# Optimization experiments

Measured on AMD Instinct MI355X. Metric: run time of the kernel, lower is better.

## Reference

```python
import jax, jax.numpy as jnp
import numpy as np

N_USERS = 100000
N_ITEMS = 50000
N = N_USERS + N_ITEMS
EMBED = 64
NNZ = 4800000
N_LAYERS = 3


def setup_inputs() -> dict:
    key = jax.random.key(0)
    k1, k2, k3, k4, k5, k6, k7 = jax.random.split(key, 7)
    adj_rows = jax.random.randint(k1, (NNZ,), 0, N, dtype=jnp.int32)
    adj_cols = jax.random.randint(k2, (NNZ,), 0, N, dtype=jnp.int32)
    # symmetric-normalized LightGCN values are small positives
    adj_vals = jax.random.uniform(k3, (NNZ,), dtype=jnp.float32) * (1.0 / 32.0)
    u_emb = jax.random.normal(k4, (N_USERS, EMBED), dtype=jnp.float32) * 0.1
    i_emb = jax.random.normal(k5, (N_ITEMS, EMBED), dtype=jnp.float32) * 0.1
    u_emb_pre = jax.random.normal(k6, (N_USERS, EMBED), dtype=jnp.float32) * 0.1
    i_emb_pre = jax.random.normal(k7, (N_ITEMS, EMBED), dtype=jnp.float32) * 0.1
    return {"adj_rows": adj_rows, "adj_cols": adj_cols, "adj_vals": adj_vals,
            "u_emb": u_emb, "i_emb": i_emb,
            "u_emb_pre": u_emb_pre, "i_emb_pre": i_emb_pre}


def _spmm(rows, cols, vals, x):
    # y = A @ x with A in COO form; gather neighbor rows, scale, scatter-add.
    gathered = x[cols] * vals[:, None]          # [nnz, d]
    return jax.ops.segment_sum(gathered, rows, num_segments=N)


def reference(adj_rows, adj_cols, adj_vals, u_emb, i_emb, u_emb_pre, i_emb_pre):
    ego = jnp.concatenate([u_emb + u_emb_pre, i_emb + i_emb_pre], axis=0)  # [N, d]
    acc = ego  # running sum instead of stacking all layer outputs
    for _ in range(N_LAYERS):
        ego = _spmm(adj_rows, adj_cols, adj_vals, ego)
        acc = acc + ego
    all_emb = acc / (N_LAYERS + 1)  # layer-wise mean
    u_g = all_emb[:N_USERS]
    i_g = all_emb[N_USERS:]
    return (u_g, i_g)
```

## Files before the change

kernel.cpp:

```cpp
#include <hip/hip_runtime.h>

#define N_USERS 100000
#define N_ITEMS 50000
#define N_NODES 150000
#define EMBED 64
#define N_LAYERS 3

#define BSH 8
#define BROWS 256
#define NB ((N_NODES + BROWS - 1) / BROWS)
#define PCHUNK 4096
#define COLMASK 0x3FFFF

__device__ __forceinline__ unsigned short f2bf(float f) {
    unsigned u = __float_as_uint(f);
    return (unsigned short)((u + 0x7FFFu + ((u >> 16) & 1u)) >> 16);
}

__global__ void lgcn_init(const float* __restrict__ u, const float* __restrict__ it,
                          const float* __restrict__ up, const float* __restrict__ ip,
                          unsigned short* __restrict__ egoh, float* __restrict__ acc) {
    int idx = blockIdx.x * blockDim.x + threadIdx.x;
    const int total = N_NODES * EMBED / 4;
    if (idx >= total) return;
    const int uCount = N_USERS * EMBED / 4;
    float4 v;
    if (idx < uCount) {
        float4 a = reinterpret_cast<const float4*>(u)[idx];
        float4 b = reinterpret_cast<const float4*>(up)[idx];
        v = make_float4(a.x + b.x, a.y + b.y, a.z + b.z, a.w + b.w);
    } else {
        int j = idx - uCount;
        float4 a = reinterpret_cast<const float4*>(it)[j];
        float4 b = reinterpret_cast<const float4*>(ip)[j];
        v = make_float4(a.x + b.x, a.y + b.y, a.z + b.z, a.w + b.w);
    }
    reinterpret_cast<float4*>(acc)[idx] = v;
    ushort4 h;
    h.x = f2bf(v.x); h.y = f2bf(v.y); h.z = f2bf(v.z); h.w = f2bf(v.w);
    reinterpret_cast<ushort4*>(egoh)[idx] = h;
}

__global__ void lgcn_cnt(const int* __restrict__ rows, int* __restrict__ Cmat, int nnz) {
    __shared__ int lcnt[NB];
    int wg = blockIdx.x;
    int c0 = wg * PCHUNK;
    int cend = min(c0 + PCHUNK, nnz);
    for (int b = threadIdx.x; b < NB; b += blockDim.x) lcnt[b] = 0;
    __syncthreads();
    for (int e = c0 + threadIdx.x; e < cend; e += blockDim.x)
        atomicAdd(&lcnt[rows[e] >> BSH], 1);
    __syncthreads();
    for (int b = threadIdx.x; b < NB; b += blockDim.x)
        Cmat[(size_t)wg * NB + b] = lcnt[b];
}

__global__ __launch_bounds__(256) void lgcn_colscan(int* __restrict__ Cmat,
                                                    int* __restrict__ colTotal, int nwg) {
    __shared__ int sm[256];
    int b = blockIdx.x;
    int carry = 0;
    for (int c0 = 0; c0 < nwg; c0 += 256) {
        int wg = c0 + threadIdx.x;
        int v = (wg < nwg) ? Cmat[(size_t)wg * NB + b] : 0;
        sm[threadIdx.x] = v;
        __syncthreads();
        for (int off = 1; off < 256; off <<= 1) {
            int t = (threadIdx.x >= (unsigned)off) ? sm[threadIdx.x - off] : 0;
            __syncthreads();
            sm[threadIdx.x] += t;
            __syncthreads();
        }
        if (wg < nwg) Cmat[(size_t)wg * NB + b] = carry + sm[threadIdx.x] - v;
        carry += sm[255];
        __syncthreads();
    }
    if (threadIdx.x == 0) colTotal[b] = carry;
}

__global__ __launch_bounds__(1024) void lgcn_btscan(const int* __restrict__ colTotal,
                                                    int* __restrict__ bucketBase,
                                                    int* __restrict__ rowptr, int nnz) {
    __shared__ int sm[1024];
    int c = (threadIdx.x < NB) ? colTotal[threadIdx.x] : 0;
    sm[threadIdx.x] = c;
    __syncthreads();
    for (int off = 1; off < 1024; off <<= 1) {
        int t = (threadIdx.x >= (unsigned)off) ? sm[threadIdx.x - off] : 0;
        __syncthreads();
        sm[threadIdx.x] += t;
        __syncthreads();
    }
    if (threadIdx.x < NB) bucketBase[threadIdx.x] = sm[threadIdx.x] - c;
    if (threadIdx.x == 0) { bucketBase[NB] = nnz; rowptr[N_NODES] = nnz; }
}

__global__ __launch_bounds__(256) void lgcn_scatter(
        const int* __restrict__ rows, const int* __restrict__ cols,
        const float* __restrict__ vals, const int* __restrict__ Cmat,
        const int* __restrict__ bucketBase, int2* __restrict__ pcvp, int nnz) {
    __shared__ int lcnt[NB];
    __shared__ int gbase[NB];
    __shared__ int sc[256];
    __shared__ int2 ebuf[PCHUNK];
    __shared__ unsigned short bbuf[PCHUNK];
    int wg = blockIdx.x;
    int c0 = wg * PCHUNK;
    int cend = min(c0 + PCHUNK, nnz);
    int n = cend - c0;

    for (int b = threadIdx.x; b < NB; b += 256) lcnt[b] = 0;
    __syncthreads();
    for (int e = c0 + threadIdx.x; e < cend; e += 256)
        atomicAdd(&lcnt[rows[e] >> BSH], 1);
    __syncthreads();

    int carry = 0;
    for (int base = 0; base < NB; base += 256) {
        int b = base + threadIdx.x;
        int v = (b < NB) ? lcnt[b] : 0;
        sc[threadIdx.x] = v;
        __syncthreads();
        for (int off = 1; off < 256; off <<= 1) {
            int t = (threadIdx.x >= (unsigned)off) ? sc[threadIdx.x - off] : 0;
            __syncthreads();
            sc[threadIdx.x] += t;
            __syncthreads();
        }
        if (b < NB) {
            int excl = carry + sc[threadIdx.x] - v;
            gbase[b] = bucketBase[b] + Cmat[(size_t)wg * NB + b] - excl;
            lcnt[b] = excl;
        }
        carry += sc[255];
        __syncthreads();
    }

    for (int e = c0 + threadIdx.x; e < cend; e += 256) {
        int r = rows[e];
        int b = r >> BSH;
        int lpos = atomicAdd(&lcnt[b], 1);
        ebuf[lpos] = make_int2(((r & (BROWS - 1)) << 18) | cols[e], __float_as_int(vals[e]));
        bbuf[lpos] = (unsigned short)b;
    }
    __syncthreads();

    for (int t = threadIdx.x; t < n; t += 256) {
        int b = bbuf[t];
        pcvp[gbase[b] + t] = ebuf[t];
    }
}

__global__ __launch_bounds__(BROWS) void lgcn_bsort(const int2* __restrict__ pcvp,
                                                    const int* __restrict__ bucketBase,
                                                    int* __restrict__ rowptr,
                                                    int2* __restrict__ cv) {
    __shared__ int sm[BROWS];
    __shared__ int cur[BROWS];
    int b = blockIdx.x;
    int beg = bucketBase[b];
    int end = bucketBase[b + 1];
    sm[threadIdx.x] = 0;
    __syncthreads();
    for (int i = beg + threadIdx.x; i < end; i += BROWS)
        atomicAdd(&sm[((unsigned)pcvp[i].x) >> 18], 1);
    __syncthreads();
    int c = sm[threadIdx.x];
    for (int off = 1; off < BROWS; off <<= 1) {
        int t = (threadIdx.x >= (unsigned)off) ? sm[threadIdx.x - off] : 0;
        __syncthreads();
        sm[threadIdx.x] += t;
        __syncthreads();
    }
    int excl = sm[threadIdx.x] - c;
    cur[threadIdx.x] = beg + excl;
    int node = b * BROWS + (int)threadIdx.x;
    if (node < N_NODES) rowptr[node] = beg + excl;
    __syncthreads();
    for (int i = beg + threadIdx.x; i < end; i += BROWS) {
        int2 p = pcvp[i];
        int rl = ((unsigned)p.x) >> 18;
        int pos = atomicAdd(&cur[rl], 1);
        cv[pos] = make_int2(p.x & COLMASK, p.y);
    }
}

template <bool WRITE_EGO>
__global__ __launch_bounds__(256) void lgcn_spmm_quad(
        const int* __restrict__ rowptr, const int2* __restrict__ cv,
        const unsigned short* __restrict__ x, unsigned short* __restrict__ ego_out,
        float* __restrict__ acc, float scale) {
    int row = blockIdx.x * 4 + (threadIdx.x >> 6);
    row = __builtin_amdgcn_readfirstlane(row);
    if (row >= N_NODES) return;
    int lane = threadIdx.x & 63;
    int grp  = lane >> 4;
    int sub  = lane & 15;
    int beg = rowptr[row];
    int end = rowptr[row + 1];

    float4 a_in = make_float4(0.f, 0.f, 0.f, 0.f);
    if (grp == 0)
        a_in = reinterpret_cast<const float4*>(acc)[(size_t)row * 16 + sub];

    float4 s = make_float4(0.f, 0.f, 0.f, 0.f);
    if (beg < end) {
        int lim = end - 1;
        int eg = grp;
        int so = sub << 2;
        int   iA = min(beg + eg, lim);
        int2  pA = cv[iA];
        float vA = (beg + eg <= lim) ? __int_as_float(pA.y) : 0.f;
        uint2 qA = *reinterpret_cast<const uint2*>(x + (((unsigned)pA.x) << 6) + so);
        int   iB = min(beg + 4 + eg, lim);
        int2  pB = cv[iB];
        float vB = (beg + 4 + eg <= lim) ? __int_as_float(pB.y) : 0.f;
        uint2 qB = *reinterpret_cast<const uint2*>(x + (((unsigned)pB.x) << 6) + so);
        for (int e = beg + 8; e < end; e += 8) {
            s.x = fmaf(vA, __uint_as_float(qA.x << 16), s.x);
            s.y = fmaf(vA, __uint_as_float(qA.x & 0xFFFF0000u), s.y);
            s.z = fmaf(vA, __uint_as_float(qA.y << 16), s.z);
            s.w = fmaf(vA, __uint_as_float(qA.y & 0xFFFF0000u), s.w);
            iA = min(e + eg, lim);
            pA = cv[iA];
            vA = (e + eg <= lim) ? __int_as_float(pA.y) : 0.f;
            qA = *reinterpret_cast<const uint2*>(x + (((unsigned)pA.x) << 6) + so);
            s.x = fmaf(vB, __uint_as_float(qB.x << 16), s.x);
            s.y = fmaf(vB, __uint_as_float(qB.x & 0xFFFF0000u), s.y);
            s.z = fmaf(vB, __uint_as_float(qB.y << 16), s.z);
            s.w = fmaf(vB, __uint_as_float(qB.y & 0xFFFF0000u), s.w);
            iB = min(e + 4 + eg, lim);
            pB = cv[iB];
            vB = (e + 4 + eg <= lim) ? __int_as_float(pB.y) : 0.f;
            qB = *reinterpret_cast<const uint2*>(x + (((unsigned)pB.x) << 6) + so);
        }
        s.x = fmaf(vA, __uint_as_float(qA.x << 16), s.x);
        s.y = fmaf(vA, __uint_as_float(qA.x & 0xFFFF0000u), s.y);
        s.z = fmaf(vA, __uint_as_float(qA.y << 16), s.z);
        s.w = fmaf(vA, __uint_as_float(qA.y & 0xFFFF0000u), s.w);
        s.x = fmaf(vB, __uint_as_float(qB.x << 16), s.x);
        s.y = fmaf(vB, __uint_as_float(qB.x & 0xFFFF0000u), s.y);
        s.z = fmaf(vB, __uint_as_float(qB.y << 16), s.z);
        s.w = fmaf(vB, __uint_as_float(qB.y & 0xFFFF0000u), s.w);
    }

    s.x += __shfl_xor(s.x, 16); s.x += __shfl_xor(s.x, 32);
    s.y += __shfl_xor(s.y, 16); s.y += __shfl_xor(s.y, 32);
    s.z += __shfl_xor(s.z, 16); s.z += __shfl_xor(s.z, 32);
    s.w += __shfl_xor(s.w, 16); s.w += __shfl_xor(s.w, 32);

    if (grp == 0) {
        size_t o4 = (size_t)row * 16 + sub;
        if (WRITE_EGO) {
            ushort4 h;
            h.x = f2bf(s.x); h.y = f2bf(s.y); h.z = f2bf(s.z); h.w = f2bf(s.w);
            reinterpret_cast<ushort4*>(ego_out)[o4] = h;
        }
        float4 r;
        r.x = (a_in.x + s.x) * scale;
        r.y = (a_in.y + s.y) * scale;
        r.z = (a_in.z + s.z) * scale;
        r.w = (a_in.w + s.w) * scale;
        reinterpret_cast<float4*>(acc)[o4] = r;
    }
}

extern "C" void kernel_launch(void* const* d_in, const int* in_sizes, int n_in,
                              void* d_out, int out_size, void* d_ws, size_t ws_size,
                              hipStream_t stream) {
    const int*   rows = (const int*)d_in[0];
    const int*   cols = (const int*)d_in[1];
    const float* vals = (const float*)d_in[2];
    const float* u    = (const float*)d_in[3];
    const float* it   = (const float*)d_in[4];
    const float* up   = (const float*)d_in[5];
    const float* ip   = (const float*)d_in[6];
    const int nnz = in_sizes[0];
    const int nwg = (nnz + PCHUNK - 1) / PCHUNK;

    float* acc = (float*)d_out;

    unsigned short* egoh0 = (unsigned short*)d_ws;
    unsigned short* egoh1 = egoh0 + (size_t)N_NODES * EMBED;
    int2*  cv         = (int2*)(egoh1 + (size_t)N_NODES * EMBED);
    int2*  pcvp       = cv + nnz;
    int*   Cmat       = (int*)(pcvp + nnz);
    int*   colTotal   = Cmat + (size_t)nwg * NB;
    int*   bucketBase = colTotal + NB;
    int*   rowptr     = bucketBase + NB + 1;

    const int tpb = 256;
    const int totalVec = N_NODES * EMBED / 4;

    lgcn_init<<<(totalVec + tpb - 1) / tpb, tpb, 0, stream>>>(u, it, up, ip, egoh0, acc);
    lgcn_cnt<<<nwg, tpb, 0, stream>>>(rows, Cmat, nnz);
    lgcn_colscan<<<NB, 256, 0, stream>>>(Cmat, colTotal, nwg);
    lgcn_btscan<<<1, 1024, 0, stream>>>(colTotal, bucketBase, rowptr, nnz);
    lgcn_scatter<<<nwg, tpb, 0, stream>>>(rows, cols, vals, Cmat, bucketBase, pcvp, nnz);
    lgcn_bsort<<<NB, BROWS, 0, stream>>>(pcvp, bucketBase, rowptr, cv);

    const int spmmBlocks = (N_NODES + 3) / 4;

    lgcn_spmm_quad<true><<<spmmBlocks, tpb, 0, stream>>>(rowptr, cv, egoh0, egoh1, acc, 1.0f);
    lgcn_spmm_quad<true><<<spmmBlocks, tpb, 0, stream>>>(rowptr, cv, egoh1, egoh0, acc, 1.0f);
    lgcn_spmm_quad<false><<<spmmBlocks, tpb, 0, stream>>>(rowptr, cv, egoh0, nullptr, acc,
                                                          1.0f / (N_LAYERS + 1));
}
```

Before: 471.0 us.

## Halve bucket size and stage bucket sort in LDS before coalesced write

Shrinks row buckets from 256 to 128 rows, which doubles the bucket count, so the bucket-total scan now loops in chunks of 1024 with a carried offset. The per-bucket sort runs with 256 threads, places entries into an LDS buffer by local row position, and then writes them to global memory contiguously. A scattered-write fallback handles buckets larger than the buffer. The aim is to replace scattered global writes with coalesced ones and to raise parallelism in the sort, at the cost of larger histogram and scan matrices in the counting stages.

```diff
diff --git a/kernel.cpp b/kernel.cpp
--- a/kernel.cpp
+++ b/kernel.cpp
@@ -6,11 +6,12 @@
 #define EMBED 64
 #define N_LAYERS 3
 
-#define BSH 8
-#define BROWS 256
+#define BSH 7
+#define BROWS 128
 #define NB ((N_NODES + BROWS - 1) / BROWS)
 #define PCHUNK 4096
 #define COLMASK 0x3FFFF
+#define CAPB 4608
 
 __device__ __forceinline__ unsigned short f2bf(float f) {
     unsigned u = __float_as_uint(f);
@@ -82,16 +83,27 @@
                                                     int* __restrict__ bucketBase,
                                                     int* __restrict__ rowptr, int nnz) {
     __shared__ int sm[1024];
-    int c = (threadIdx.x < NB) ? colTotal[threadIdx.x] : 0;
-    sm[threadIdx.x] = c;
-    __syncthreads();
-    for (int off = 1; off < 1024; off <<= 1) {
-        int t = (threadIdx.x >= (unsigned)off) ? sm[threadIdx.x - off] : 0;
-        __syncthreads();
-        sm[threadIdx.x] += t;
-        __syncthreads();
-    }
-    if (threadIdx.x < NB) bucketBase[threadIdx.x] = sm[threadIdx.x] - c;
+    __shared__ int carry_s;
+    if (threadIdx.x == 0) carry_s = 0;
+    __syncthreads();
+    for (int base = 0; base < NB; base += 1024) {
+        int i = base + threadIdx.x;
+        int c = (i < NB) ? colTotal[i] : 0;
+        sm[threadIdx.x] = c;
+        __syncthreads();
+        for (int off = 1; off < 1024; off <<= 1) {
+            int t = (threadIdx.x >= (unsigned)off) ? sm[threadIdx.x - off] : 0;
+            __syncthreads();
+            sm[threadIdx.x] += t;
+            __syncthreads();
+        }
+        int r0 = carry_s;
+        if (i < NB) bucketBase[i] = r0 + sm[threadIdx.x] - c;
+        int tot = sm[1023];
+        __syncthreads();
+        if (threadIdx.x == 0) carry_s = r0 + tot;
+        __syncthreads();
+    }
     if (threadIdx.x == 0) { bucketBase[NB] = nnz; rowptr[N_NODES] = nnz; }
 }
 
@@ -151,37 +163,57 @@
     }
 }
 
-__global__ __launch_bounds__(BROWS) void lgcn_bsort(const int2* __restrict__ pcvp,
-                                                    const int* __restrict__ bucketBase,
-                                                    int* __restrict__ rowptr,
-                                                    int2* __restrict__ cv) {
+__global__ __launch_bounds__(256) void lgcn_bsort(const int2* __restrict__ pcvp,
+                                                  const int* __restrict__ bucketBase,
+                                                  int* __restrict__ rowptr,
+                                                  int2* __restrict__ cv) {
     __shared__ int sm[BROWS];
     __shared__ int cur[BROWS];
+    __shared__ int2 sbuf[CAPB];
     int b = blockIdx.x;
     int beg = bucketBase[b];
     int end = bucketBase[b + 1];
-    sm[threadIdx.x] = 0;
-    __syncthreads();
-    for (int i = beg + threadIdx.x; i < end; i += BROWS)
+    int n = end - beg;
+
+    if (threadIdx.x < BROWS) sm[threadIdx.x] = 0;
+    __syncthreads();
+    for (int i = beg + threadIdx.x; i < end; i += 256)
         atomicAdd(&sm[((unsigned)pcvp[i].x) >> 18], 1);
     __syncthreads();
-    int c = sm[threadIdx.x];
+
+    int c = (threadIdx.x < BROWS) ? sm[threadIdx.x] : 0;
     for (int off = 1; off < BROWS; off <<= 1) {
-        int t = (threadIdx.x >= (unsigned)off) ? sm[threadIdx.x - off] : 0;
-        __syncthreads();
-        sm[threadIdx.x] += t;
-        __syncthreads();
-    }
-    int excl = sm[threadIdx.x] - c;
-    cur[threadIdx.x] = beg + excl;
-    int node = b * BROWS + (int)threadIdx.x;
-    if (node < N_NODES) rowptr[node] = beg + excl;
-    __syncthreads();
-    for (int i = beg + threadIdx.x; i < end; i += BROWS) {
-        int2 p = pcvp[i];
-        int rl = ((unsigned)p.x) >> 18;
-        int pos = atomicAdd(&cur[rl], 1);
-        cv[pos] = make_int2(p.x & COLMASK, p.y);
+        int t = (threadIdx.x < BROWS && threadIdx.x >= (unsigned)off)
+                    ? sm[threadIdx.x - off] : 0;
+        __syncthreads();
+        if (threadIdx.x < BROWS) sm[threadIdx.x] += t;
+        __syncthreads();
+    }
+    if (threadIdx.x < BROWS) {
+        int excl = sm[threadIdx.x] - c;
+        cur[threadIdx.x] = excl;
+        int node = b * BROWS + (int)threadIdx.x;
+        if (node < N_NODES) rowptr[node] = beg + excl;
+    }
+    __syncthreads();
+
+    if (n <= CAPB) {
+        for (int i = beg + threadIdx.x; i < end; i += 256) {
+            int2 p = pcvp[i];
+            int rl = ((unsigned)p.x) >> 18;
+            int lpos = atomicAdd(&cur[rl], 1);
+            sbuf[lpos] = make_int2(p.x & COLMASK, p.y);
+        }
+        __syncthreads();
+        for (int t = threadIdx.x; t < n; t += 256)
+            cv[beg + t] = sbuf[t];
+    } else {
+        for (int i = beg + threadIdx.x; i < end; i += 256) {
+            int2 p = pcvp[i];
+            int rl = ((unsigned)p.x) >> 18;
+            int pos = atomicAdd(&cur[rl], 1);
+            cv[beg + pos] = make_int2(p.x & COLMASK, p.y);
+        }
     }
 }
 
@@ -297,7 +329,7 @@
     lgcn_colscan<<<NB, 256, 0, stream>>>(Cmat, colTotal, nwg);
     lgcn_btscan<<<1, 1024, 0, stream>>>(colTotal, bucketBase, rowptr, nnz);
     lgcn_scatter<<<nwg, tpb, 0, stream>>>(rows, cols, vals, Cmat, bucketBase, pcvp, nnz);
-    lgcn_bsort<<<NB, BROWS, 0, stream>>>(pcvp, bucketBase, rowptr, cv);
+    lgcn_bsort<<<NB, 256, 0, stream>>>(pcvp, bucketBase, rowptr, cv);
 
     const int spmmBlocks = (N_NODES + 3) / 4;
 
```

Result: no change. 472.2 us (+0.3%).
